# Kernel tuning notes

Measured on AMD Instinct MI355X. Metric: run time of the kernel, lower is better.

## Reference

```python
import jax, jax.numpy as jnp
import numpy as np

T, D, E, K = 16384, 2048, 64, 2
LOAD_BALANCE_SCALE = 0.01
NOISY_STD = 1.0


def setup_inputs() -> dict:
    key = jax.random.key(0)
    k1, k2, k3, k4 = jax.random.split(key, 4)
    x_flat = jax.random.normal(k1, (T, D), dtype=jnp.float32)
    noise = jax.random.normal(k2, (T, E), dtype=jnp.float32)
    # gate_linear: nn.Linear(D, E, bias=False) -> weight [E, D]
    W_gate = jax.random.normal(k3, (E, D), dtype=jnp.float32) * (1.0 / np.sqrt(D))
    # noise_weight initialized to zeros in torch; use small values so the
    # noisy path is exercised numerically.
    noise_weight = jax.random.normal(k4, (E,), dtype=jnp.float32) * 0.01
    return {"x_flat": x_flat, "noise": noise, "W_gate": W_gate,
            "noise_weight": noise_weight, "k": K}


def reference(x_flat, noise, W_gate, noise_weight, k):
    # logits = x @ W^T   [T, E]
    logits = jnp.einsum("td,ed->te", x_flat, W_gate)
    logits_noisy = logits + (noise * NOISY_STD) * noise_weight

    # noisy top-k; softmax over -inf-sparse logits == softmax over the k
    # selected logits scattered into zeros (top-k ids are unique per row).
    top_vals, top_ids = jax.lax.top_k(logits_noisy, k)          # [T, k]
    gates_k = jax.nn.softmax(top_vals, axis=-1)                 # [T, k]
    rows = jnp.arange(x_flat.shape[0])[:, None]
    top_k_gated_weights = jnp.zeros_like(logits_noisy).at[rows, top_ids].set(gates_k)

    # load-balance loss on clean logits
    gate_weights_mean = jax.nn.softmax(logits, axis=-1).mean(axis=0)  # [E]
    uniform = jnp.full_like(gate_weights_mean, 1.0 / gate_weights_mean.shape[0])
    load_balance_loss = jnp.mean((gate_weights_mean - uniform) ** 2) * LOAD_BALANCE_SCALE

    return top_k_gated_weights, top_ids, load_balance_loss
```

## Files before the change

kernel.cpp:

```cpp
#include <hip/hip_runtime.h>
#include <hip/hip_bf16.h>

#define T_TOK 16384
#define D_DIM 2048
#define E_EXP 64
#define TAU   2e-3f

typedef __bf16 bf16x8 __attribute__((ext_vector_type(8)));
typedef float  f32x16 __attribute__((ext_vector_type(16)));
typedef unsigned short ushort_t;

#define WS_WHI  0
#define WS_WLO  (256*1024)
#define WS_SUM  (512*1024)
#define WS_CNT  (512*1024 + 512)
#define WS_FLG  (512*1024 + 1024)

__device__ __forceinline__ unsigned short bf16_rne(float x){
  unsigned int u = __float_as_uint(x);
  return (unsigned short)((u + 0x7FFFu + ((u >> 16) & 1u)) >> 16);
}

__device__ __forceinline__ void ins3(float& v1, int& i1, float& v2, int& i2,
                                     float& v3, int& i3, float v, int i){
  if (v > v1 || (v == v1 && i < i1)) { v3=v2; i3=i2; v2=v1; i2=i1; v1=v; i1=i; }
  else if (v > v2 || (v == v2 && i < i2)) { v3=v2; i3=i2; v2=v; i2=i; }
  else if (v > v3 || (v == v3 && i < i3)) { v3=v; i3=i; }
}

__device__ __forceinline__ void gload16(const void* g, const void* l){
  __builtin_amdgcn_global_load_lds(
      (const __attribute__((address_space(1))) unsigned int*)g,
      (__attribute__((address_space(3))) unsigned int*)l, 16, 0, 0);
}

__global__ void wsplit_kernel(const float* __restrict__ W,
                              ushort_t* __restrict__ whi, ushort_t* __restrict__ wlo,
                              double* __restrict__ ESUM, int* __restrict__ FCNT){
  const int n = blockIdx.x * 256 + threadIdx.x;
  if (blockIdx.x == 0){
    if (threadIdx.x < 64) ESUM[threadIdx.x] = 0.0;
    else if (threadIdx.x == 64) *FCNT = 0;
  }
  const int lane = n & 63;
  const int eh   = (n >> 6) & 1;
  const int t    = (n >> 7) & 7;
  const int c    = n >> 10;
  const float* src = W + (size_t)(eh*32 + (lane & 31))*D_DIM
                       + c*128 + t*16 + (lane >> 5)*8;
  float4 w0 = *reinterpret_cast<const float4*>(src);
  float4 w1 = *reinterpret_cast<const float4*>(src + 4);
  float f[8] = {w0.x,w0.y,w0.z,w0.w,w1.x,w1.y,w1.z,w1.w};
  unsigned h[8], lo[8];
  #pragma unroll
  for (int i = 0; i < 8; ++i){
    h[i]  = bf16_rne(f[i]);
    lo[i] = bf16_rne(f[i] - __uint_as_float(h[i] << 16));
  }
  uint4 hv = { h[0]|(h[1]<<16),  h[2]|(h[3]<<16),  h[4]|(h[5]<<16),  h[6]|(h[7]<<16) };
  uint4 lv = { lo[0]|(lo[1]<<16), lo[2]|(lo[3]<<16), lo[4]|(lo[5]<<16), lo[6]|(lo[7]<<16) };
  *reinterpret_cast<uint4*>(whi + (size_t)n*8) = hv;
  *reinterpret_cast<uint4*>(wlo + (size_t)n*8) = lv;
}

__launch_bounds__(512, 4)
__global__ void moe_main(const float* __restrict__ X, const float* __restrict__ NZ,
                         const ushort_t* __restrict__ WHI, const ushort_t* __restrict__ WLO,
                         const float* __restrict__ NW, float* __restrict__ OUT,
                         double* __restrict__ ESUM, int* __restrict__ FCNT,
                         int* __restrict__ FLIST)
{
  __shared__ __align__(16) char smem[32768];

  const int tid  = threadIdx.x;
  const int lane = tid & 63;
  const int wv   = tid >> 6;
  const int eh   = wv & 1;
  const int ks   = wv >> 1;
  const int r0   = blockIdx.x << 5;
  const int m    = lane & 31;
  const int kg   = lane >> 5;

  const int n0   = wv*64 + lane;
  const int row0 = n0 >> 5, g0 = n0 & 31;
  const int gs0  = (g0 & 24) | ((g0 ^ row0) & 7);
  const char* px0 = (const char*)X + ((size_t)(r0 + row0)*D_DIM + gs0*4) * 4;
  const char* px1 = px0 + (size_t)16*D_DIM*4;
  const char* ldsx0 = smem +        wv*1024;
  const char* ldsx1 = smem + 8192 + wv*1024;

  const char* pwh = (const char*)WHI + (size_t)(ks*256 + eh*64 + lane)*16;
  const char* pwl = (const char*)WLO + (size_t)(ks*256 + eh*64 + lane)*16;

  const int gf0 = ks*8 + kg*2;
  const int gf1 = gf0 + 4;
  const int offA0 = m*512 + (((gf0  ) & 24) | (((gf0  ) ^ m) & 7))*16;
  const int offB0 = m*512 + (((gf0+1) & 24) | (((gf0+1) ^ m) & 7))*16;
  const int offA1 = m*512 + (((gf1  ) & 24) | (((gf1  ) ^ m) & 7))*16;
  const int offB1 = m*512 + (((gf1+1) & 24) | (((gf1+1) ^ m) & 7))*16;

  f32x16 acc;
  #pragma unroll
  for (int i = 0; i < 16; ++i) acc[i] = 0.0f;

  uint4 whA0, wlA0, whA1, wlA1;
  uint4 whB0, wlB0, whB1, wlB1;

  #define LOADW(c, H0, L0, H1, L1) do{                                         \
    H0 = *reinterpret_cast<const uint4*>(pwh + (size_t)(c)*16384);             \
    L0 = *reinterpret_cast<const uint4*>(pwl + (size_t)(c)*16384);             \
    H1 = *reinterpret_cast<const uint4*>(pwh + (size_t)(c)*16384 + 2048);      \
    L1 = *reinterpret_cast<const uint4*>(pwl + (size_t)(c)*16384 + 2048);      \
  }while(0)

  #define ISSUE(c, BUF, H0, L0, H1, L1) do{                                    \
    __builtin_amdgcn_sched_barrier(0);                                         \
    gload16(px0 + (size_t)(c)*512, ldsx0 + (BUF));                             \
    gload16(px1 + (size_t)(c)*512, ldsx1 + (BUF));                             \
    LOADW(c, H0, L0, H1, L1);                                                  \
    __builtin_amdgcn_sched_barrier(0);                                         \
  }while(0)

  #define CVT8(fa, fb, ah, al) do{                                             \
    float fv[8] = {fa.x,fa.y,fa.z,fa.w,fb.x,fb.y,fb.z,fb.w};                   \
    _Pragma("unroll")                                                          \
    for (int ii = 0; ii < 8; ++ii){                                            \
      __bf16 hh = (__bf16)fv[ii];                                              \
      ah[ii] = hh; al[ii] = (__bf16)(fv[ii] - (float)hh);                      \
    }                                                                          \
  }while(0)

  #define KS2(BUF, OA, OB, WH, WL) do{                                         \
    float4 fa = *reinterpret_cast<const float4*>(smem + (BUF) + (OA));         \
    float4 fb = *reinterpret_cast<const float4*>(smem + (BUF) + (OB));         \
    bf16x8 ah, al;                                                             \
    CVT8(fa, fb, ah, al);                                                      \
    bf16x8 bh = __builtin_bit_cast(bf16x8, WH);                                \
    bf16x8 bl = __builtin_bit_cast(bf16x8, WL);                                \
    acc = __builtin_amdgcn_mfma_f32_32x32x16_bf16(ah, bh, acc, 0, 0, 0);       \
    acc = __builtin_amdgcn_mfma_f32_32x32x16_bf16(ah, bl, acc, 0, 0, 0);       \
    acc = __builtin_amdgcn_mfma_f32_32x32x16_bf16(al, bh, acc, 0, 0, 0);       \
  }while(0)

  #define PHASE(cc, H0, L0, H1, L1, BUF, WNTOK, DOISS) do{                     \
    asm volatile("s_waitcnt vmcnt(" WNTOK ")" ::: "memory");                   \
    __builtin_amdgcn_sched_barrier(0);                                         \
    __builtin_amdgcn_s_barrier();                                              \
    KS2(BUF, offA0, offB0, H0, L0);                                            \
    KS2(BUF, offA1, offB1, H1, L1);                                            \
    __builtin_amdgcn_s_barrier();                                              \
    if (DOISS) ISSUE((cc) + 2, BUF, H0, L0, H1, L1);                           \
  }while(0)

  ISSUE(0, 0,     whA0, wlA0, whA1, wlA1);
  ISSUE(1, 16384, whB0, wlB0, whB1, wlB1);

  #pragma unroll 1
  for (int g = 0; g < 7; ++g){
    PHASE(2*g,     whA0, wlA0, whA1, wlA1, 0,     "6", 1);
    PHASE(2*g + 1, whB0, wlB0, whB1, wlB1, 16384, "6", 1);
  }
  PHASE(14, whA0, wlA0, whA1, wlA1, 0,     "6", 0);
  PHASE(15, whB0, wlB0, whB1, wlB1, 16384, "0", 0);

  #undef PHASE
  #undef KS2
  #undef CVT8
  #undef ISSUE
  #undef LOADW

  float* lgts = (float*)(smem);
  float* nzs  = (float*)(smem + 8192);
  float* prb  = (float*)(smem + 16384);
  float* nws  = (float*)(smem + 24576);
  const int ex = eh*32 + m;

  __syncthreads();
  if (ks == 0){
    #pragma unroll
    for (int r = 0; r < 16; ++r){
      int rr = (r & 3) + ((r >> 2) << 3) + (kg << 2);
      lgts[rr*64 + ex] = acc[r];
    }
  }
  __syncthreads();
  #pragma unroll
  for (int p = 1; p < 4; ++p){
    if (ks == p){
      #pragma unroll
      for (int r = 0; r < 16; ++r){
        int rr = (r & 3) + ((r >> 2) << 3) + (kg << 2);
        lgts[rr*64 + ex] += acc[r];
      }
    }
    __syncthreads();
  }

  const int sr = tid >> 4, sc = tid & 15;
  *reinterpret_cast<float4*>(&nzs[sr*64 + sc*4]) =
    *reinterpret_cast<const float4*>(NZ + (size_t)(r0 + sr)*E_EXP + sc*4);
  if (tid < 64) nws[tid] = NW[tid];
  __syncthreads();

  if (wv < 4){
    const int rrow = (wv << 3) + (lane >> 3);
    const int j    = lane & 7;
    const int trow = r0 + rrow;
    float cl[8];
    float v1 = -INFINITY, v2 = -INFINITY, v3 = -INFINITY;
    int   i1 = 1 << 29,   i2 = 1 << 29,   i3 = 1 << 29;
    #pragma unroll
    for (int mm = 0; mm < 8; ++mm){
      int q = j + (mm << 3);
      float lg = lgts[rrow*64 + q];
      cl[mm] = lg;
      float vn = fmaf(nzs[rrow*64 + q], nws[q], lg);
      ins3(v1,i1,v2,i2,v3,i3, vn, q);
    }
    #pragma unroll
    for (int d = 1; d < 8; d <<= 1){
      float ov1 = __shfl_xor(v1, d, 8), ov2 = __shfl_xor(v2, d, 8), ov3 = __shfl_xor(v3, d, 8);
      int   oi1 = __shfl_xor(i1, d, 8), oi2 = __shfl_xor(i2, d, 8), oi3 = __shfl_xor(i3, d, 8);
      ins3(v1,i1,v2,i2,v3,i3, ov1, oi1);
      ins3(v1,i1,v2,i2,v3,i3, ov2, oi2);
      ins3(v1,i1,v2,i2,v3,i3, ov3, oi3);
    }
    float e1 = expf(v2 - v1);
    float g0g = 1.0f / (1.0f + e1);
    float g1g = e1 * g0g;

    float mx = cl[0];
    #pragma unroll
    for (int mm = 1; mm < 8; ++mm) mx = fmaxf(mx, cl[mm]);
    #pragma unroll
    for (int d = 1; d < 8; d <<= 1) mx = fmaxf(mx, __shfl_xor(mx, d, 8));
    float sum = 0.0f, exv[8];
    #pragma unroll
    for (int mm = 0; mm < 8; ++mm){ exv[mm] = expf(cl[mm] - mx); sum += exv[mm]; }
    #pragma unroll
    for (int d = 1; d < 8; d <<= 1) sum += __shfl_xor(sum, d, 8);
    float inv = 1.0f / sum;
    #pragma unroll
    for (int mm = 0; mm < 8; ++mm) prb[rrow*64 + j + (mm << 3)] = exv[mm] * inv;

    if (j == 0){
      OUT[(size_t)T_TOK*E_EXP + (size_t)trow*2]     = (float)i1;
      OUT[(size_t)T_TOK*E_EXP + (size_t)trow*2 + 1] = (float)i2;
      if ((v1 - v2 < TAU) || (v2 - v3 < TAU)){
        int slot = atomicAdd(FCNT, 1);
        FLIST[slot] = trow;
      }
    }
    #pragma unroll
    for (int mm = 0; mm < 8; ++mm){
      int q = j + (mm << 3);
      lgts[rrow*64 + q] = (q == i1) ? g0g : ((q == i2) ? g1g : 0.0f);
    }
  }
  __syncthreads();

  *reinterpret_cast<float4*>(OUT + (size_t)(r0 + sr)*E_EXP + sc*4) =
    *reinterpret_cast<const float4*>(&lgts[sr*64 + sc*4]);
  if (tid < 64){
    float s0 = 0.0f;
    #pragma unroll 8
    for (int rr2 = 0; rr2 < 32; ++rr2) s0 += prb[rr2*64 + tid];
    atomicAdd(&ESUM[tid], (double)s0);
  }
}

__launch_bounds__(256)
__global__ void moe_fixup(const float* __restrict__ X, const float* __restrict__ NZ,
                          const float* __restrict__ WG, const float* __restrict__ NW,
                          float* __restrict__ OUT, const int* __restrict__ FCNT,
                          const int* __restrict__ FLIST)
{
  __shared__ __align__(16) float xl[2048];
  __shared__ double lz[64];
  __shared__ int   si1, si2;
  __shared__ float sg0, sg1;
  const int n    = *FCNT;
  const int lane = threadIdx.x & 63;
  const int wv   = threadIdx.x >> 6;
  for (int idx = blockIdx.x; idx < n; idx += gridDim.x){
    const int t = FLIST[idx];
    {
      int off = threadIdx.x * 8;
      *reinterpret_cast<float4*>(xl + off) =
        *reinterpret_cast<const float4*>(X + (size_t)t*D_DIM + off);
      *reinterpret_cast<float4*>(xl + off + 4) =
        *reinterpret_cast<const float4*>(X + (size_t)t*D_DIM + off + 4);
    }
    __syncthreads();
    for (int s = 0; s < 16; ++s){
      const int e = wv*16 + s;
      const float* wr = WG + (size_t)e*D_DIM;
      double acc = 0.0;
      #pragma unroll
      for (int it = 0; it < 8; ++it){
        float4 w4 = *reinterpret_cast<const float4*>(wr + it*256 + lane*4);
        float4 x4 = *reinterpret_cast<const float4*>(xl + it*256 + lane*4);
        acc += (double)x4.x * (double)w4.x;
        acc += (double)x4.y * (double)w4.y;
        acc += (double)x4.z * (double)w4.z;
        acc += (double)x4.w * (double)w4.w;
      }
      #pragma unroll
      for (int off = 1; off < 64; off <<= 1) acc += __shfl_xor(acc, off, 64);
      if (lane == 0)
        lz[e] = acc + (double)NZ[(size_t)t*E_EXP + e] * (double)NW[e];
    }
    __syncthreads();
    if (threadIdx.x == 0){
      double b1 = -1e300, b2 = -1e300; int j1 = 0, j2 = 0;
      for (int q = 0; q < 64; ++q){
        double v = lz[q];
        if (v > b1){ b2 = b1; j2 = j1; b1 = v; j1 = q; }
        else if (v > b2){ b2 = v; j2 = q; }
      }
      double ee = exp(b2 - b1);
      sg0 = (float)(1.0 / (1.0 + ee));
      sg1 = (float)(ee / (1.0 + ee));
      si1 = j1; si2 = j2;
      OUT[(size_t)T_TOK*E_EXP + (size_t)t*2]     = (float)j1;
      OUT[(size_t)T_TOK*E_EXP + (size_t)t*2 + 1] = (float)j2;
    }
    __syncthreads();
    if (threadIdx.x < 64)
      OUT[(size_t)t*E_EXP + threadIdx.x] = (threadIdx.x == si1) ? sg0 :
                                           ((threadIdx.x == si2) ? sg1 : 0.0f);
    __syncthreads();
  }
}

__global__ void moe_loss(const double* __restrict__ ESUM, float* __restrict__ OUT){
  const int e = threadIdx.x;
  double d = ESUM[e] * (1.0 / T_TOK) - (1.0 / 64.0);
  double sq = d * d;
  #pragma unroll
  for (int off = 1; off < 64; off <<= 1) sq += __shfl_xor(sq, off, 64);
  if (e == 0) OUT[(size_t)T_TOK*E_EXP + T_TOK*2] = (float)(sq * (0.01 / 64.0));
}

extern "C" void kernel_launch(void* const* d_in, const int* in_sizes, int n_in,
                              void* d_out, int out_size, void* d_ws, size_t ws_size,
                              hipStream_t stream)
{
  const float* X  = (const float*)d_in[0];
  const float* NZ = (const float*)d_in[1];
  const float* WG = (const float*)d_in[2];
  const float* NW = (const float*)d_in[3];
  float* OUT = (float*)d_out;
  char*  ws  = (char*)d_ws;
  ushort_t* WHI = (ushort_t*)(ws + WS_WHI);
  ushort_t* WLO = (ushort_t*)(ws + WS_WLO);
  double* ESUM = (double*)(ws + WS_SUM);
  int* FCNT  = (int*)(ws + WS_CNT);
  int* FLIST = (int*)(ws + WS_FLG);

  wsplit_kernel<<<dim3(64), dim3(256), 0, stream>>>(WG, WHI, WLO, ESUM, FCNT);
  moe_main<<<dim3(T_TOK/32), dim3(512), 0, stream>>>(X, NZ, WHI, WLO, NW, OUT, ESUM, FCNT, FLIST);
  moe_fixup<<<dim3(512), dim3(256), 0, stream>>>(X, NZ, WG, NW, OUT, FCNT, FLIST);
  moe_loss<<<dim3(1), dim3(64), 0, stream>>>(ESUM, OUT);
}
```

Baseline: 113.1 us.

## Double token tile to 64 rows per block and split K across two wave groups

Each block now processes 64 token rows instead of 32, and its 8 waves split into two M-halves by two K-halves instead of one M tile by four K-slices. The weight layout in the split kernel is reshaped to match, so every weight fragment loaded to registers is reused across more rows. The cross-wave reduction drops from four serialized passes to a single add. In exchange LDS per block doubles to about 64KB, launch bounds drop to one block per SM hint, and the grid halves, which lowers occupancy and latency hiding.

```diff
diff --git a/kernel.cpp b/kernel.cpp
--- a/kernel.cpp
+++ b/kernel.cpp
@@ -42,12 +42,9 @@
     if (threadIdx.x < 64) ESUM[threadIdx.x] = 0.0;
     else if (threadIdx.x == 64) *FCNT = 0;
   }
-  const int lane = n & 63;
-  const int eh   = (n >> 6) & 1;
-  const int t    = (n >> 7) & 7;
-  const int c    = n >> 10;
-  const float* src = W + (size_t)(eh*32 + (lane & 31))*D_DIM
-                       + c*128 + t*16 + (lane >> 5)*8;
+  const int e  = n >> 8;
+  const int k0 = (n & 255) * 8;
+  const float* src = W + (size_t)e*D_DIM + k0;
   float4 w0 = *reinterpret_cast<const float4*>(src);
   float4 w1 = *reinterpret_cast<const float4*>(src + 4);
   float f[8] = {w0.x,w0.y,w0.z,w0.w,w1.x,w1.y,w1.z,w1.w};
@@ -59,82 +56,87 @@
   }
   uint4 hv = { h[0]|(h[1]<<16),  h[2]|(h[3]<<16),  h[4]|(h[5]<<16),  h[6]|(h[7]<<16) };
   uint4 lv = { lo[0]|(lo[1]<<16), lo[2]|(lo[3]<<16), lo[4]|(lo[5]<<16), lo[6]|(lo[7]<<16) };
-  *reinterpret_cast<uint4*>(whi + (size_t)n*8) = hv;
-  *reinterpret_cast<uint4*>(wlo + (size_t)n*8) = lv;
-}
-
-__launch_bounds__(512, 4)
+  const int c  = k0 >> 7, ks = (k0 >> 6) & 1, t = (k0 >> 4) & 3, kg = (k0 >> 3) & 1;
+  const int gidx = c*1024 + ks*512 + t*128 + (e >> 5)*64 + kg*32 + (e & 31);
+  *reinterpret_cast<uint4*>(whi + (size_t)gidx*8) = hv;
+  *reinterpret_cast<uint4*>(wlo + (size_t)gidx*8) = lv;
+}
+
+__launch_bounds__(512, 1)
 __global__ void moe_main(const float* __restrict__ X, const float* __restrict__ NZ,
                          const ushort_t* __restrict__ WHI, const ushort_t* __restrict__ WLO,
                          const float* __restrict__ NW, float* __restrict__ OUT,
                          double* __restrict__ ESUM, int* __restrict__ FCNT,
                          int* __restrict__ FLIST)
 {
-  __shared__ __align__(16) char smem[32768];
+  __shared__ __align__(16) char smem[65792];
 
   const int tid  = threadIdx.x;
   const int lane = tid & 63;
   const int wv   = tid >> 6;
   const int eh   = wv & 1;
-  const int ks   = wv >> 1;
-  const int r0   = blockIdx.x << 5;
+  const int ks   = (wv >> 1) & 1;
+  const int mh   = wv >> 2;
+  const int r0   = blockIdx.x << 6;
   const int m    = lane & 31;
   const int kg   = lane >> 5;
-
-  const int n0   = wv*64 + lane;
-  const int row0 = n0 >> 5, g0 = n0 & 31;
-  const int gs0  = (g0 & 24) | ((g0 ^ row0) & 7);
-  const char* px0 = (const char*)X + ((size_t)(r0 + row0)*D_DIM + gs0*4) * 4;
-  const char* px1 = px0 + (size_t)16*D_DIM*4;
-  const char* ldsx0 = smem +        wv*1024;
-  const char* ldsx1 = smem + 8192 + wv*1024;
-
-  const char* pwh = (const char*)WHI + (size_t)(ks*256 + eh*64 + lane)*16;
-  const char* pwl = (const char*)WLO + (size_t)(ks*256 + eh*64 + lane)*16;
-
-  const int gf0 = ks*8 + kg*2;
-  const int gf1 = gf0 + 4;
-  const int offA0 = m*512 + (((gf0  ) & 24) | (((gf0  ) ^ m) & 7))*16;
-  const int offB0 = m*512 + (((gf0+1) & 24) | (((gf0+1) ^ m) & 7))*16;
-  const int offA1 = m*512 + (((gf1  ) & 24) | (((gf1  ) ^ m) & 7))*16;
-  const int offB1 = m*512 + (((gf1+1) & 24) | (((gf1+1) ^ m) & 7))*16;
+  const int row  = mh*32 + m;
+
+  const char* pq[4];
+  #pragma unroll
+  for (int q = 0; q < 4; ++q){
+    const int rw = wv*8 + q*2 + (lane >> 5);
+    const int gp = lane & 31;
+    const int g  = (gp & 24) | ((gp ^ rw) & 7);
+    pq[q] = (const char*)X + ((size_t)(r0 + rw)*D_DIM + g*4) * 4;
+  }
+  const char* pq0 = pq[0]; const char* pq1 = pq[1];
+  const char* pq2 = pq[2]; const char* pq3 = pq[3];
+
+  const char* pwh = (const char*)WHI + (size_t)(ks*512 + eh*64 + lane)*16;
+  const char* pwl = (const char*)WLO + (size_t)(ks*512 + eh*64 + lane)*16;
+
+  #define XOFF(t, h) (row*512 + ((((ks*16 + (t)*4 + kg*2 + (h)) & 24) | (((ks*16 + (t)*4 + kg*2 + (h)) ^ row) & 7)) << 4))
+  const int xo00 = XOFF(0,0), xo01 = XOFF(0,1);
+  const int xo10 = XOFF(1,0), xo11 = XOFF(1,1);
+  const int xo20 = XOFF(2,0), xo21 = XOFF(2,1);
+  const int xo30 = XOFF(3,0), xo31 = XOFF(3,1);
+  #undef XOFF
 
   f32x16 acc;
   #pragma unroll
   for (int i = 0; i < 16; ++i) acc[i] = 0.0f;
 
-  uint4 whA0, wlA0, whA1, wlA1;
-  uint4 whB0, wlB0, whB1, wlB1;
-
-  #define LOADW(c, H0, L0, H1, L1) do{                                         \
+  uint4 hA0,lA0,hA1,lA1,hA2,lA2,hA3,lA3;
+  uint4 hB0,lB0,hB1,lB1,hB2,lB2,hB3,lB3;
+
+  #define ISSUE(c, BUF, H0,L0,H1,L1,H2,L2,H3,L3) do{                           \
+    __builtin_amdgcn_sched_barrier(0);                                         \
+    gload16(pq0 + (size_t)(c)*512, smem + (BUF) + wv*4096);                    \
+    gload16(pq1 + (size_t)(c)*512, smem + (BUF) + wv*4096 + 1024);             \
+    gload16(pq2 + (size_t)(c)*512, smem + (BUF) + wv*4096 + 2048);             \
+    gload16(pq3 + (size_t)(c)*512, smem + (BUF) + wv*4096 + 3072);             \
     H0 = *reinterpret_cast<const uint4*>(pwh + (size_t)(c)*16384);             \
     L0 = *reinterpret_cast<const uint4*>(pwl + (size_t)(c)*16384);             \
     H1 = *reinterpret_cast<const uint4*>(pwh + (size_t)(c)*16384 + 2048);      \
     L1 = *reinterpret_cast<const uint4*>(pwl + (size_t)(c)*16384 + 2048);      \
-  }while(0)
-
-  #define ISSUE(c, BUF, H0, L0, H1, L1) do{                                    \
-    __builtin_amdgcn_sched_barrier(0);                                         \
-    gload16(px0 + (size_t)(c)*512, ldsx0 + (BUF));                             \
-    gload16(px1 + (size_t)(c)*512, ldsx1 + (BUF));                             \
-    LOADW(c, H0, L0, H1, L1);                                                  \
+    H2 = *reinterpret_cast<const uint4*>(pwh + (size_t)(c)*16384 + 4096);      \
+    L2 = *reinterpret_cast<const uint4*>(pwl + (size_t)(c)*16384 + 4096);      \
+    H3 = *reinterpret_cast<const uint4*>(pwh + (size_t)(c)*16384 + 6144);      \
+    L3 = *reinterpret_cast<const uint4*>(pwl + (size_t)(c)*16384 + 6144);      \
     __builtin_amdgcn_sched_barrier(0);                                         \
   }while(0)
 
-  #define CVT8(fa, fb, ah, al) do{                                             \
-    float fv[8] = {fa.x,fa.y,fa.z,fa.w,fb.x,fb.y,fb.z,fb.w};                   \
-    _Pragma("unroll")                                                          \
-    for (int ii = 0; ii < 8; ++ii){                                            \
-      __bf16 hh = (__bf16)fv[ii];                                              \
-      ah[ii] = hh; al[ii] = (__bf16)(fv[ii] - (float)hh);                      \
-    }                                                                          \
-  }while(0)
-
-  #define KS2(BUF, OA, OB, WH, WL) do{                                         \
+  #define KSTEP(BUF, OA, OB, WH, WL) do{                                       \
     float4 fa = *reinterpret_cast<const float4*>(smem + (BUF) + (OA));         \
     float4 fb = *reinterpret_cast<const float4*>(smem + (BUF) + (OB));         \
     bf16x8 ah, al;                                                             \
-    CVT8(fa, fb, ah, al);                                                      \
+    { float fv[8] = {fa.x,fa.y,fa.z,fa.w,fb.x,fb.y,fb.z,fb.w};                 \
+      _Pragma("unroll")                                                        \
+      for (int ii = 0; ii < 8; ++ii){                                          \
+        __bf16 hh = (__bf16)fv[ii];                                            \
+        ah[ii] = hh; al[ii] = (__bf16)(fv[ii] - (float)hh);                    \
+      } }                                                                      \
     bf16x8 bh = __builtin_bit_cast(bf16x8, WH);                                \
     bf16x8 bl = __builtin_bit_cast(bf16x8, WL);                                \
     acc = __builtin_amdgcn_mfma_f32_32x32x16_bf16(ah, bh, acc, 0, 0, 0);       \
@@ -142,67 +144,77 @@
     acc = __builtin_amdgcn_mfma_f32_32x32x16_bf16(al, bh, acc, 0, 0, 0);       \
   }while(0)
 
-  #define PHASE(cc, H0, L0, H1, L1, BUF, WNTOK, DOISS) do{                     \
-    asm volatile("s_waitcnt vmcnt(" WNTOK ")" ::: "memory");                   \
-    __builtin_amdgcn_sched_barrier(0);                                         \
-    __builtin_amdgcn_s_barrier();                                              \
-    KS2(BUF, offA0, offB0, H0, L0);                                            \
-    KS2(BUF, offA1, offB1, H1, L1);                                            \
-    __builtin_amdgcn_s_barrier();                                              \
-    if (DOISS) ISSUE((cc) + 2, BUF, H0, L0, H1, L1);                           \
+  #define COMPUTE(BUF, H0,L0,H1,L1,H2,L2,H3,L3) do{                            \
+    KSTEP(BUF, xo00, xo01, H0, L0);                                            \
+    KSTEP(BUF, xo10, xo11, H1, L1);                                            \
+    KSTEP(BUF, xo20, xo21, H2, L2);                                            \
+    KSTEP(BUF, xo30, xo31, H3, L3);                                            \
   }while(0)
 
-  ISSUE(0, 0,     whA0, wlA0, whA1, wlA1);
-  ISSUE(1, 16384, whB0, wlB0, whB1, wlB1);
+  #define WAITV(N) do{ asm volatile("s_waitcnt vmcnt(" #N ")" ::: "memory");   \
+                       __builtin_amdgcn_sched_barrier(0); }while(0)
+
+  ISSUE(0, 0,     hA0,lA0,hA1,lA1,hA2,lA2,hA3,lA3);
+  ISSUE(1, 32768, hB0,lB0,hB1,lB1,hB2,lB2,hB3,lB3);
 
   #pragma unroll 1
   for (int g = 0; g < 7; ++g){
-    PHASE(2*g,     whA0, wlA0, whA1, wlA1, 0,     "6", 1);
-    PHASE(2*g + 1, whB0, wlB0, whB1, wlB1, 16384, "6", 1);
-  }
-  PHASE(14, whA0, wlA0, whA1, wlA1, 0,     "6", 0);
-  PHASE(15, whB0, wlB0, whB1, wlB1, 16384, "0", 0);
-
-  #undef PHASE
-  #undef KS2
-  #undef CVT8
+    const int c = 2*g;
+    WAITV(12); __builtin_amdgcn_s_barrier();
+    COMPUTE(0, hA0,lA0,hA1,lA1,hA2,lA2,hA3,lA3);
+    __builtin_amdgcn_s_barrier();
+    ISSUE(c+2, 0, hA0,lA0,hA1,lA1,hA2,lA2,hA3,lA3);
+    WAITV(12); __builtin_amdgcn_s_barrier();
+    COMPUTE(32768, hB0,lB0,hB1,lB1,hB2,lB2,hB3,lB3);
+    __builtin_amdgcn_s_barrier();
+    ISSUE(c+3, 32768, hB0,lB0,hB1,lB1,hB2,lB2,hB3,lB3);
+  }
+  WAITV(12); __builtin_amdgcn_s_barrier();
+  COMPUTE(0, hA0,lA0,hA1,lA1,hA2,lA2,hA3,lA3);
+  __builtin_amdgcn_s_barrier();
+  WAITV(0);  __builtin_amdgcn_s_barrier();
+  COMPUTE(32768, hB0,lB0,hB1,lB1,hB2,lB2,hB3,lB3);
+
   #undef ISSUE
-  #undef LOADW
+  #undef KSTEP
+  #undef COMPUTE
+  #undef WAITV
 
   float* lgts = (float*)(smem);
-  float* nzs  = (float*)(smem + 8192);
-  float* prb  = (float*)(smem + 16384);
-  float* nws  = (float*)(smem + 24576);
+  float* nzs  = (float*)(smem + 16384);
+  float* prb  = (float*)(smem + 32768);
+  float* red  = (float*)(smem + 49152);
+  float* nws  = (float*)(smem + 65536);
   const int ex = eh*32 + m;
 
+  __syncthreads();
+  if (ks == 1){
+    #pragma unroll
+    for (int r = 0; r < 16; ++r){
+      int rr = (r & 3) + ((r >> 2) << 3) + (kg << 2);
+      red[(mh*32 + rr)*64 + ex] = acc[r];
+    }
+  }
   __syncthreads();
   if (ks == 0){
     #pragma unroll
     for (int r = 0; r < 16; ++r){
       int rr = (r & 3) + ((r >> 2) << 3) + (kg << 2);
-      lgts[rr*64 + ex] = acc[r];
-    }
-  }
-  __syncthreads();
-  #pragma unroll
-  for (int p = 1; p < 4; ++p){
-    if (ks == p){
-      #pragma unroll
-      for (int r = 0; r < 16; ++r){
-        int rr = (r & 3) + ((r >> 2) << 3) + (kg << 2);
-        lgts[rr*64 + ex] += acc[r];
-      }
-    }
-    __syncthreads();
-  }
-
-  const int sr = tid >> 4, sc = tid & 15;
-  *reinterpret_cast<float4*>(&nzs[sr*64 + sc*4]) =
-    *reinterpret_cast<const float4*>(NZ + (size_t)(r0 + sr)*E_EXP + sc*4);
+      int idx = (mh*32 + rr)*64 + ex;
+      lgts[idx] = acc[r] + red[idx];
+    }
+  }
+  {
+    const int rw = tid >> 3, cb = (tid & 7) * 8;
+    *reinterpret_cast<float4*>(&nzs[rw*64 + cb]) =
+      *reinterpret_cast<const float4*>(NZ + (size_t)(r0 + rw)*E_EXP + cb);
+    *reinterpret_cast<float4*>(&nzs[rw*64 + cb + 4]) =
+      *reinterpret_cast<const float4*>(NZ + (size_t)(r0 + rw)*E_EXP + cb + 4);
+  }
   if (tid < 64) nws[tid] = NW[tid];
   __syncthreads();
 
-  if (wv < 4){
+  {
     const int rrow = (wv << 3) + (lane >> 3);
     const int j    = lane & 7;
     const int trow = r0 + rrow;
@@ -259,12 +271,17 @@
   }
   __syncthreads();
 
-  *reinterpret_cast<float4*>(OUT + (size_t)(r0 + sr)*E_EXP + sc*4) =
-    *reinterpret_cast<const float4*>(&lgts[sr*64 + sc*4]);
+  {
+    const int rw = tid >> 3, cb = (tid & 7) * 8;
+    *reinterpret_cast<float4*>(OUT + (size_t)(r0 + rw)*E_EXP + cb) =
+      *reinterpret_cast<const float4*>(&lgts[rw*64 + cb]);
+    *reinterpret_cast<float4*>(OUT + (size_t)(r0 + rw)*E_EXP + cb + 4) =
+      *reinterpret_cast<const float4*>(&lgts[rw*64 + cb + 4]);
+  }
   if (tid < 64){
     float s0 = 0.0f;
     #pragma unroll 8
-    for (int rr2 = 0; rr2 < 32; ++rr2) s0 += prb[rr2*64 + tid];
+    for (int rr2 = 0; rr2 < 64; ++rr2) s0 += prb[rr2*64 + tid];
     atomicAdd(&ESUM[tid], (double)s0);
   }
 }
@@ -359,7 +376,7 @@
   int* FLIST = (int*)(ws + WS_FLG);
 
   wsplit_kernel<<<dim3(64), dim3(256), 0, stream>>>(WG, WHI, WLO, ESUM, FCNT);
-  moe_main<<<dim3(T_TOK/32), dim3(512), 0, stream>>>(X, NZ, WHI, WLO, NW, OUT, ESUM, FCNT, FLIST);
+  moe_main<<<dim3(T_TOK/64), dim3(512), 0, stream>>>(X, NZ, WHI, WLO, NW, OUT, ESUM, FCNT, FLIST);
   moe_fixup<<<dim3(512), dim3(256), 0, stream>>>(X, NZ, WG, NW, OUT, FCNT, FLIST);
   moe_loss<<<dim3(1), dim3(64), 0, stream>>>(ESUM, OUT);
 }
```

Result: faster. 105.6 us (-6.7%).

## Replace global atomics with per-block partials and flags, merge loss into fixup

Applied to the files above, without the earlier changes.

Global atomic work goes away. The main kernel writes per-block partial softmax sums and a per-token ambiguity flag, where before it did double-precision atomicAdds to a global sum and an atomic counter plus a compacted list. A single finalize kernel now has one block reduce the partials into the load-balance loss while the other 512 blocks each scan their 32 tokens' flags and recompute the flagged ones. This removes atomic contention, the zero-init step and one kernel launch. In exchange the fixup blocks must read flags for every token, and flagged tokens are no longer spread evenly across the grid.

```diff
diff --git a/kernel.cpp b/kernel.cpp
--- a/kernel.cpp
+++ b/kernel.cpp
@@ -12,9 +12,8 @@
 
 #define WS_WHI  0
 #define WS_WLO  (256*1024)
-#define WS_SUM  (512*1024)
-#define WS_CNT  (512*1024 + 512)
-#define WS_FLG  (512*1024 + 1024)
+#define WS_PART (512*1024)
+#define WS_FLAG (640*1024)
 
 __device__ __forceinline__ unsigned short bf16_rne(float x){
   unsigned int u = __float_as_uint(x);
@@ -35,19 +34,14 @@
 }
 
 __global__ void wsplit_kernel(const float* __restrict__ W,
-                              ushort_t* __restrict__ whi, ushort_t* __restrict__ wlo,
-                              double* __restrict__ ESUM, int* __restrict__ FCNT){
+                              ushort_t* __restrict__ whi, ushort_t* __restrict__ wlo){
   const int n = blockIdx.x * 256 + threadIdx.x;
-  if (blockIdx.x == 0){
-    if (threadIdx.x < 64) ESUM[threadIdx.x] = 0.0;
-    else if (threadIdx.x == 64) *FCNT = 0;
-  }
   const int lane = n & 63;
   const int eh   = (n >> 6) & 1;
-  const int t    = (n >> 7) & 7;
+  const int w    = (n >> 7) & 7;
   const int c    = n >> 10;
   const float* src = W + (size_t)(eh*32 + (lane & 31))*D_DIM
-                       + c*128 + t*16 + (lane >> 5)*8;
+                       + c*128 + w*16 + (lane >> 5)*8;
   float4 w0 = *reinterpret_cast<const float4*>(src);
   float4 w1 = *reinterpret_cast<const float4*>(src + 4);
   float f[8] = {w0.x,w0.y,w0.z,w0.w,w1.x,w1.y,w1.z,w1.w};
@@ -67,8 +61,7 @@
 __global__ void moe_main(const float* __restrict__ X, const float* __restrict__ NZ,
                          const ushort_t* __restrict__ WHI, const ushort_t* __restrict__ WLO,
                          const float* __restrict__ NW, float* __restrict__ OUT,
-                         double* __restrict__ ESUM, int* __restrict__ FCNT,
-                         int* __restrict__ FLIST)
+                         float* __restrict__ PART, int* __restrict__ FLAG)
 {
   __shared__ __align__(16) char smem[32768];
 
@@ -246,10 +239,7 @@
     if (j == 0){
       OUT[(size_t)T_TOK*E_EXP + (size_t)trow*2]     = (float)i1;
       OUT[(size_t)T_TOK*E_EXP + (size_t)trow*2 + 1] = (float)i2;
-      if ((v1 - v2 < TAU) || (v2 - v3 < TAU)){
-        int slot = atomicAdd(FCNT, 1);
-        FLIST[slot] = trow;
-      }
+      FLAG[trow] = ((v1 - v2 < TAU) || (v2 - v3 < TAU)) ? 1 : 0;
     }
     #pragma unroll
     for (int mm = 0; mm < 8; ++mm){
@@ -265,25 +255,46 @@
     float s0 = 0.0f;
     #pragma unroll 8
     for (int rr2 = 0; rr2 < 32; ++rr2) s0 += prb[rr2*64 + tid];
-    atomicAdd(&ESUM[tid], (double)s0);
+    PART[(size_t)blockIdx.x*64 + tid] = s0;
   }
 }
 
 __launch_bounds__(256)
-__global__ void moe_fixup(const float* __restrict__ X, const float* __restrict__ NZ,
-                          const float* __restrict__ WG, const float* __restrict__ NW,
-                          float* __restrict__ OUT, const int* __restrict__ FCNT,
-                          const int* __restrict__ FLIST)
+__global__ void moe_finalize(const float* __restrict__ X, const float* __restrict__ NZ,
+                             const float* __restrict__ WG, const float* __restrict__ NW,
+                             float* __restrict__ OUT, const float* __restrict__ PART,
+                             const int* __restrict__ FLAG)
 {
   __shared__ __align__(16) float xl[2048];
   __shared__ double lz[64];
+  __shared__ double ps[4][64];
   __shared__ int   si1, si2;
   __shared__ float sg0, sg1;
-  const int n    = *FCNT;
+
+  if (blockIdx.x == 0){
+    const int e = threadIdx.x & 63;
+    const int p = threadIdx.x >> 6;
+    double s = 0.0;
+    for (int b = p; b < 512; b += 4) s += (double)PART[(size_t)b*64 + e];
+    ps[p][e] = s;
+    __syncthreads();
+    if (threadIdx.x < 64){
+      double tot = ps[0][e] + ps[1][e] + ps[2][e] + ps[3][e];
+      double d = tot * (1.0 / T_TOK) - (1.0 / 64.0);
+      double sq = d * d;
+      #pragma unroll
+      for (int off = 1; off < 64; off <<= 1) sq += __shfl_xor(sq, off, 64);
+      if (e == 0) OUT[(size_t)T_TOK*E_EXP + T_TOK*2] = (float)(sq * (0.01 / 64.0));
+    }
+    return;
+  }
+
+  const int r0   = (blockIdx.x - 1) * 32;
   const int lane = threadIdx.x & 63;
   const int wv   = threadIdx.x >> 6;
-  for (int idx = blockIdx.x; idx < n; idx += gridDim.x){
-    const int t = FLIST[idx];
+  for (int i = 0; i < 32; ++i){
+    const int t = r0 + i;
+    if (FLAG[t] == 0) continue;
     {
       int off = threadIdx.x * 8;
       *reinterpret_cast<float4*>(xl + off) =
@@ -333,15 +344,6 @@
   }
 }
 
-__global__ void moe_loss(const double* __restrict__ ESUM, float* __restrict__ OUT){
-  const int e = threadIdx.x;
-  double d = ESUM[e] * (1.0 / T_TOK) - (1.0 / 64.0);
-  double sq = d * d;
-  #pragma unroll
-  for (int off = 1; off < 64; off <<= 1) sq += __shfl_xor(sq, off, 64);
-  if (e == 0) OUT[(size_t)T_TOK*E_EXP + T_TOK*2] = (float)(sq * (0.01 / 64.0));
-}
-
 extern "C" void kernel_launch(void* const* d_in, const int* in_sizes, int n_in,
                               void* d_out, int out_size, void* d_ws, size_t ws_size,
                               hipStream_t stream)
@@ -354,12 +356,10 @@
   char*  ws  = (char*)d_ws;
   ushort_t* WHI = (ushort_t*)(ws + WS_WHI);
   ushort_t* WLO = (ushort_t*)(ws + WS_WLO);
-  double* ESUM = (double*)(ws + WS_SUM);
-  int* FCNT  = (int*)(ws + WS_CNT);
-  int* FLIST = (int*)(ws + WS_FLG);
-
-  wsplit_kernel<<<dim3(64), dim3(256), 0, stream>>>(WG, WHI, WLO, ESUM, FCNT);
-  moe_main<<<dim3(T_TOK/32), dim3(512), 0, stream>>>(X, NZ, WHI, WLO, NW, OUT, ESUM, FCNT, FLIST);
-  moe_fixup<<<dim3(512), dim3(256), 0, stream>>>(X, NZ, WG, NW, OUT, FCNT, FLIST);
-  moe_loss<<<dim3(1), dim3(64), 0, stream>>>(ESUM, OUT);
-}
+  float* PART = (float*)(ws + WS_PART);
+  int*   FLAG = (int*)(ws + WS_FLAG);
+
+  wsplit_kernel<<<dim3(64), dim3(256), 0, stream>>>(WG, WHI, WLO);
+  moe_main<<<dim3(T_TOK/32), dim3(512), 0, stream>>>(X, NZ, WHI, WLO, NW, OUT, PART, FLAG);
+  moe_finalize<<<dim3(513), dim3(256), 0, stream>>>(X, NZ, WG, NW, OUT, PART, FLAG);
+}
```

Result: slower. 196.5 us (+73.7%).

## Fuse near-tie fixup and loss reduction into main kernel, drop two launches

Applied to the files above, without the earlier changes.

Moves the fp64 recompute for near-tie tokens into the tail of the main kernel, using a per-block shared flag array in place of a global atomic list. The final load-balance loss is computed by the last block to finish, detected with a done-counter atomic. The weight-split kernel now reads the weight rows coalesced and scatters its writes into the same swizzled layout. This removes two kernel launches and the global flag list, at the cost of extra shared-memory use and serial per-block fixup work inside the main kernel.

```diff
diff --git a/kernel.cpp b/kernel.cpp
--- a/kernel.cpp
+++ b/kernel.cpp
@@ -13,8 +13,7 @@
 #define WS_WHI  0
 #define WS_WLO  (256*1024)
 #define WS_SUM  (512*1024)
-#define WS_CNT  (512*1024 + 512)
-#define WS_FLG  (512*1024 + 1024)
+#define WS_DONE (512*1024 + 512)
 
 __device__ __forceinline__ unsigned short bf16_rne(float x){
   unsigned int u = __float_as_uint(x);
@@ -36,18 +35,15 @@
 
 __global__ void wsplit_kernel(const float* __restrict__ W,
                               ushort_t* __restrict__ whi, ushort_t* __restrict__ wlo,
-                              double* __restrict__ ESUM, int* __restrict__ FCNT){
-  const int n = blockIdx.x * 256 + threadIdx.x;
-  if (blockIdx.x == 0){
-    if (threadIdx.x < 64) ESUM[threadIdx.x] = 0.0;
-    else if (threadIdx.x == 64) *FCNT = 0;
-  }
-  const int lane = n & 63;
-  const int eh   = (n >> 6) & 1;
-  const int t    = (n >> 7) & 7;
-  const int c    = n >> 10;
-  const float* src = W + (size_t)(eh*32 + (lane & 31))*D_DIM
-                       + c*128 + t*16 + (lane >> 5)*8;
+                              double* __restrict__ ESUM, int* __restrict__ DONE){
+  const int t = threadIdx.x;
+  const int e = blockIdx.x;
+  if (e == 0){
+    if (t < 64) ESUM[t] = 0.0;
+    else if (t == 64) *DONE = 0;
+  }
+  const int k0 = t * 8;
+  const float* src = W + (size_t)e*D_DIM + k0;
   float4 w0 = *reinterpret_cast<const float4*>(src);
   float4 w1 = *reinterpret_cast<const float4*>(src + 4);
   float f[8] = {w0.x,w0.y,w0.z,w0.w,w1.x,w1.y,w1.z,w1.w};
@@ -59,16 +55,21 @@
   }
   uint4 hv = { h[0]|(h[1]<<16),  h[2]|(h[3]<<16),  h[4]|(h[5]<<16),  h[6]|(h[7]<<16) };
   uint4 lv = { lo[0]|(lo[1]<<16), lo[2]|(lo[3]<<16), lo[4]|(lo[5]<<16), lo[6]|(lo[7]<<16) };
-  *reinterpret_cast<uint4*>(whi + (size_t)n*8) = hv;
-  *reinterpret_cast<uint4*>(wlo + (size_t)n*8) = lv;
+  const int eh = e >> 5, m = e & 31;
+  const int c  = k0 >> 7;
+  const int w  = (k0 >> 4) & 7;
+  const int kg = (k0 >> 3) & 1;
+  const int G  = c*1024 + w*128 + eh*64 + kg*32 + m;
+  *reinterpret_cast<uint4*>(whi + (size_t)G*8) = hv;
+  *reinterpret_cast<uint4*>(wlo + (size_t)G*8) = lv;
 }
 
 __launch_bounds__(512, 4)
 __global__ void moe_main(const float* __restrict__ X, const float* __restrict__ NZ,
                          const ushort_t* __restrict__ WHI, const ushort_t* __restrict__ WLO,
-                         const float* __restrict__ NW, float* __restrict__ OUT,
-                         double* __restrict__ ESUM, int* __restrict__ FCNT,
-                         int* __restrict__ FLIST)
+                         const float* __restrict__ NW, const float* __restrict__ WG,
+                         float* __restrict__ OUT, double* __restrict__ ESUM,
+                         int* __restrict__ DONE)
 {
   __shared__ __align__(16) char smem[32768];
 
@@ -173,6 +174,11 @@
   float* nzs  = (float*)(smem + 8192);
   float* prb  = (float*)(smem + 16384);
   float* nws  = (float*)(smem + 24576);
+  int*   flg  = (int*)(smem + 24832);
+  double* lz  = (double*)(smem + 25088);
+  int*   sfi  = (int*)(smem + 25600);
+  float* sfg  = (float*)(smem + 25616);
+  int*   stk  = (int*)(smem + 25632);
   const int ex = eh*32 + m;
 
   __syncthreads();
@@ -246,10 +252,7 @@
     if (j == 0){
       OUT[(size_t)T_TOK*E_EXP + (size_t)trow*2]     = (float)i1;
       OUT[(size_t)T_TOK*E_EXP + (size_t)trow*2 + 1] = (float)i2;
-      if ((v1 - v2 < TAU) || (v2 - v3 < TAU)){
-        int slot = atomicAdd(FCNT, 1);
-        FLIST[slot] = trow;
-      }
+      flg[rrow] = ((v1 - v2 < TAU) || (v2 - v3 < TAU)) ? 1 : 0;
     }
     #pragma unroll
     for (int mm = 0; mm < 8; ++mm){
@@ -267,51 +270,38 @@
     for (int rr2 = 0; rr2 < 32; ++rr2) s0 += prb[rr2*64 + tid];
     atomicAdd(&ESUM[tid], (double)s0);
   }
-}
-
-__launch_bounds__(256)
-__global__ void moe_fixup(const float* __restrict__ X, const float* __restrict__ NZ,
-                          const float* __restrict__ WG, const float* __restrict__ NW,
-                          float* __restrict__ OUT, const int* __restrict__ FCNT,
-                          const int* __restrict__ FLIST)
-{
-  __shared__ __align__(16) float xl[2048];
-  __shared__ double lz[64];
-  __shared__ int   si1, si2;
-  __shared__ float sg0, sg1;
-  const int n    = *FCNT;
-  const int lane = threadIdx.x & 63;
-  const int wv   = threadIdx.x >> 6;
-  for (int idx = blockIdx.x; idx < n; idx += gridDim.x){
-    const int t = FLIST[idx];
+  __syncthreads();
+
+  float* xl = (float*)(smem + 16384);
+  for (int rloc = 0; rloc < 32; ++rloc){
+    if (flg[rloc] == 0) continue;
+    const int t = r0 + rloc;
     {
-      int off = threadIdx.x * 8;
+      int off = tid * 4;
       *reinterpret_cast<float4*>(xl + off) =
         *reinterpret_cast<const float4*>(X + (size_t)t*D_DIM + off);
-      *reinterpret_cast<float4*>(xl + off + 4) =
-        *reinterpret_cast<const float4*>(X + (size_t)t*D_DIM + off + 4);
-    }
-    __syncthreads();
-    for (int s = 0; s < 16; ++s){
-      const int e = wv*16 + s;
+    }
+    __syncthreads();
+    for (int s = 0; s < 8; ++s){
+      const int e = wv*8 + s;
       const float* wr = WG + (size_t)e*D_DIM;
-      double acc = 0.0;
+      double accd = 0.0;
       #pragma unroll
       for (int it = 0; it < 8; ++it){
         float4 w4 = *reinterpret_cast<const float4*>(wr + it*256 + lane*4);
         float4 x4 = *reinterpret_cast<const float4*>(xl + it*256 + lane*4);
-        acc += (double)x4.x * (double)w4.x;
-        acc += (double)x4.y * (double)w4.y;
-        acc += (double)x4.z * (double)w4.z;
-        acc += (double)x4.w * (double)w4.w;
+        accd += (double)x4.x * (double)w4.x;
+        accd += (double)x4.y * (double)w4.y;
+        accd += (double)x4.z * (double)w4.z;
+        accd += (double)x4.w * (double)w4.w;
       }
       #pragma unroll
-      for (int off = 1; off < 64; off <<= 1) acc += __shfl_xor(acc, off, 64);
+      for (int off = 1; off < 64; off <<= 1) accd += __shfl_xor(accd, off, 64);
       if (lane == 0)
-        lz[e] = acc + (double)NZ[(size_t)t*E_EXP + e] * (double)NW[e];
-    }
-    __syncthreads();
-    if (threadIdx.x == 0){
+        lz[e] = accd + (double)NZ[(size_t)t*E_EXP + e] * (double)NW[e];
+    }
+    __syncthreads();
+    if (tid == 0){
       double b1 = -1e300, b2 = -1e300; int j1 = 0, j2 = 0;
       for (int q = 0; q < 64; ++q){
         double v = lz[q];
@@ -319,27 +309,34 @@
         else if (v > b2){ b2 = v; j2 = q; }
       }
       double ee = exp(b2 - b1);
-      sg0 = (float)(1.0 / (1.0 + ee));
-      sg1 = (float)(ee / (1.0 + ee));
-      si1 = j1; si2 = j2;
+      sfg[0] = (float)(1.0 / (1.0 + ee));
+      sfg[1] = (float)(ee / (1.0 + ee));
+      sfi[0] = j1; sfi[1] = j2;
       OUT[(size_t)T_TOK*E_EXP + (size_t)t*2]     = (float)j1;
       OUT[(size_t)T_TOK*E_EXP + (size_t)t*2 + 1] = (float)j2;
     }
     __syncthreads();
-    if (threadIdx.x < 64)
-      OUT[(size_t)t*E_EXP + threadIdx.x] = (threadIdx.x == si1) ? sg0 :
-                                           ((threadIdx.x == si2) ? sg1 : 0.0f);
-    __syncthreads();
-  }
-}
-
-__global__ void moe_loss(const double* __restrict__ ESUM, float* __restrict__ OUT){
-  const int e = threadIdx.x;
-  double d = ESUM[e] * (1.0 / T_TOK) - (1.0 / 64.0);
-  double sq = d * d;
-  #pragma unroll
-  for (int off = 1; off < 64; off <<= 1) sq += __shfl_xor(sq, off, 64);
-  if (e == 0) OUT[(size_t)T_TOK*E_EXP + T_TOK*2] = (float)(sq * (0.01 / 64.0));
+    if (tid < 64)
+      OUT[(size_t)t*E_EXP + tid] = (tid == sfi[0]) ? sfg[0] :
+                                   ((tid == sfi[1]) ? sfg[1] : 0.0f);
+    __syncthreads();
+  }
+
+  if (tid == 0){
+    __threadfence();
+    *stk = atomicAdd(DONE, 1);
+  }
+  __syncthreads();
+  if (*stk == (int)gridDim.x - 1){
+    if (tid < 64){
+      double v = atomicAdd(&ESUM[tid], 0.0);
+      double d = v * (1.0 / T_TOK) - (1.0 / 64.0);
+      double sq = d * d;
+      #pragma unroll
+      for (int off = 1; off < 64; off <<= 1) sq += __shfl_xor(sq, off, 64);
+      if (tid == 0) OUT[(size_t)T_TOK*E_EXP + T_TOK*2] = (float)(sq * (0.01 / 64.0));
+    }
+  }
 }
 
 extern "C" void kernel_launch(void* const* d_in, const int* in_sizes, int n_in,
@@ -355,11 +352,9 @@
   ushort_t* WHI = (ushort_t*)(ws + WS_WHI);
   ushort_t* WLO = (ushort_t*)(ws + WS_WLO);
   double* ESUM = (double*)(ws + WS_SUM);
-  int* FCNT  = (int*)(ws + WS_CNT);
-  int* FLIST = (int*)(ws + WS_FLG);
-
-  wsplit_kernel<<<dim3(64), dim3(256), 0, stream>>>(WG, WHI, WLO, ESUM, FCNT);
-  moe_main<<<dim3(T_TOK/32), dim3(512), 0, stream>>>(X, NZ, WHI, WLO, NW, OUT, ESUM, FCNT, FLIST);
-  moe_fixup<<<dim3(512), dim3(256), 0, stream>>>(X, NZ, WG, NW, OUT, FCNT, FLIST);
-  moe_loss<<<dim3(1), dim3(64), 0, stream>>>(ESUM, OUT);
-}
+  int*   DONE  = (int*)(ws + WS_DONE);
+
+  wsplit_kernel<<<dim3(64), dim3(256), 0, stream>>>(WG, WHI, WLO, ESUM, DONE);
+  moe_main<<<dim3(T_TOK/32), dim3(512), 0, stream>>>(X, NZ, WHI, WLO, NW, WG,
+                                                     OUT, ESUM, DONE);
+}
```

Measured after the change: 154.2 us. 1.36x slower.
